# Kernel optimization log

Measured on AMD Instinct MI355X. Metric: run time of the kernel, lower is better.

The kernel has to match this reference:

```python
import jax, jax.numpy as jnp
import numpy as np

N = 50000
EPS = 1e-5


def gcn_conv(x, W, b, src, dst, n):
    # x: [n, Cin]; W: [Cin, Cout]; src/dst: [E+n] with self-loops included
    h = x @ W  # dense GEMM
    deg = jax.ops.segment_sum(jnp.ones_like(dst, dtype=h.dtype), dst, num_segments=n)
    dinv = jnp.where(deg > 0, jax.lax.rsqrt(deg), 0.0)
    norm = dinv[src] * dinv[dst]  # [E+n]
    msgs = h[src] * norm[:, None]  # gather + scale
    out = jax.ops.segment_sum(msgs, dst, num_segments=n)  # scatter-add
    return out + b


def batch_norm(x, gamma, beta, mean, var):
    return (x - mean) * jax.lax.rsqrt(var + EPS) * gamma + beta


def setup_inputs() -> dict:
    key = jax.random.key(0)
    ks = jax.random.split(key, 16)
    IN, H, OUT, E = 1280, 256, 500, 1600000
    x = jax.random.normal(ks[0], (N, IN), dtype=jnp.float32)
    edge_index = jax.random.randint(ks[1], (2, E), 0, N, dtype=jnp.int64)
    def lin(k, cin, cout):
        return jax.random.normal(k, (cin, cout), dtype=jnp.float32) / np.sqrt(cin)
    return {
        "x": x,
        "edge_index": edge_index,
        "W1": lin(ks[2], IN, H), "b1": jnp.zeros((H,), jnp.float32),
        "g1": jnp.ones((H,), jnp.float32), "be1": jnp.zeros((H,), jnp.float32),
        "m1": 0.1 * jax.random.normal(ks[3], (H,), jnp.float32),
        "v1": 0.5 + jax.random.uniform(ks[4], (H,), jnp.float32),
        "W2": lin(ks[5], H, H), "b2": jnp.zeros((H,), jnp.float32),
        "g2": jnp.ones((H,), jnp.float32), "be2": jnp.zeros((H,), jnp.float32),
        "m2": 0.1 * jax.random.normal(ks[6], (H,), jnp.float32),
        "v2": 0.5 + jax.random.uniform(ks[7], (H,), jnp.float32),
        "W3": lin(ks[8], H, OUT), "b3": jnp.zeros((OUT,), jnp.float32),
    }


def reference(x, edge_index, W1, b1, g1, be1, m1, v1, W2, b2, g2, be2, m2, v2, W3, b3):
    n = x.shape[0]
    loops = jnp.arange(n, dtype=edge_index.dtype)
    src = jnp.concatenate([edge_index[0], loops])
    dst = jnp.concatenate([edge_index[1], loops])
    h = gcn_conv(x, W1, b1, src, dst, n)
    h = jax.nn.relu(batch_norm(h, g1, be1, m1, v1))
    h = gcn_conv(h, W2, b2, src, dst, n)
    h = jax.nn.relu(batch_norm(h, g2, be2, m2, v2))
    return gcn_conv(h, W3, b3, src, dst, n)
```

## Files before the change

### kernel.cpp

```cpp
#include <hip/hip_runtime.h>
#include <hip/hip_bf16.h>
#include <stdint.h>

typedef __attribute__((ext_vector_type(4))) float f32x4;
typedef __attribute__((ext_vector_type(8))) short s16x8;
typedef __attribute__((ext_vector_type(4))) unsigned short u16x4;

#define EPSBN 1e-5f

__device__ __forceinline__ float bf2f(unsigned short u) {
  union { unsigned int i; float f; } w; w.i = ((unsigned int)u) << 16; return w.f;
}
__device__ __forceinline__ unsigned short f2bf(float f) {
  __hip_bfloat16 h = __float2bfloat16(f);
  unsigned short u; __builtin_memcpy(&u, &h, 2); return u;
}
__device__ __forceinline__ void gld_lds16(const void* g, void* l) {
  __builtin_amdgcn_global_load_lds(
      (const __attribute__((address_space(1))) void*)(g),
      (__attribute__((address_space(3))) void*)(l), 16, 0, 0);
}

__global__ void k_count(const int* __restrict__ dst, unsigned* __restrict__ deg, int E) {
  int i = blockIdx.x * 256 + threadIdx.x;
  if (i < E) atomicAdd(&deg[dst[i]], 1u);
}
__global__ void k_prep2(const unsigned* __restrict__ deg, float* __restrict__ dinv,
                        unsigned* __restrict__ bsum, int n) {
  __shared__ unsigned s[256];
  int t = threadIdx.x, i = blockIdx.x * 256 + t;
  unsigned d = (i < n) ? deg[i] + 1u : 0u;
  if (i < n) dinv[i] = rsqrtf((float)d);
  s[t] = d;
  __syncthreads();
  for (int st = 128; st > 0; st >>= 1) {
    if (t < st) s[t] += s[t + st];
    __syncthreads();
  }
  if (t == 0) bsum[blockIdx.x] = s[0];
}
__global__ void k_scan_top(const unsigned* __restrict__ bsum, unsigned* __restrict__ bpre,
                           int nb, unsigned* __restrict__ offs, int n) {
  __shared__ unsigned s[256];
  int t = threadIdx.x;
  unsigned v = (t < nb) ? bsum[t] : 0u;
  s[t] = v; __syncthreads();
  for (int d = 1; d < 256; d <<= 1) {
    unsigned a = (t >= d) ? s[t - d] : 0u;
    __syncthreads();
    s[t] += a;
    __syncthreads();
  }
  bpre[t] = s[t] - v;
  if (t == 255) offs[n] = s[255];
}
__global__ void k_scan_fin(const unsigned* __restrict__ deg, const unsigned* __restrict__ bpre,
                           unsigned* __restrict__ offs, unsigned* __restrict__ cur, int n) {
  __shared__ unsigned s[256];
  int t = threadIdx.x, i = blockIdx.x * 256 + t;
  unsigned v = (i < n) ? deg[i] + 1u : 0u;
  s[t] = v; __syncthreads();
  for (int d = 1; d < 256; d <<= 1) {
    unsigned a = (t >= d) ? s[t - d] : 0u;
    __syncthreads();
    s[t] += a;
    __syncthreads();
  }
  if (i < n) {
    unsigned o = bpre[blockIdx.x] + s[t] - v;
    offs[i] = o; cur[i] = o;
  }
}
__global__ void k_fill(const int* __restrict__ src, const int* __restrict__ dst,
                       unsigned* __restrict__ cur, unsigned short* __restrict__ ewp,
                       int E, int n) {
  int i = blockIdx.x * 256 + threadIdx.x;
  int s, d;
  if (i < E)          { s = src[i]; d = dst[i]; }
  else if (i < E + n) { s = d = i - E; }
  else return;
  unsigned p = atomicAdd(&cur[d], 1u);
  ewp[p] = (unsigned short)s;
}
__global__ __launch_bounds__(256) void k_sortw(const unsigned* __restrict__ offs,
                                               unsigned short* __restrict__ ewp, int nN) {
  int wv = (blockIdx.x * 256 + threadIdx.x) >> 6;
  int lane = threadIdx.x & 63;
  if (wv >= nN) return;
  unsigned beg = offs[wv], end = offs[wv + 1];
  int len = (int)(end - beg);
  if (len > 64) return;
  int k = (lane < len) ? (int)ewp[beg + lane] : 0x10000;
#pragma unroll
  for (int size = 2; size <= 64; size <<= 1) {
#pragma unroll
    for (int stride = size >> 1; stride > 0; stride >>= 1) {
      int other = __shfl_xor(k, stride);
      bool up = (lane & size) == 0;
      bool lower = (lane & stride) == 0;
      k = (lower == up) ? min(k, other) : max(k, other);
    }
  }
  if (lane < len) ewp[beg + lane] = (unsigned short)k;
}
__global__ void k_wt3(const float* __restrict__ W1, unsigned short* __restrict__ Wt1,
                      const float* __restrict__ W2, unsigned short* __restrict__ Wt2,
                      const float* __restrict__ W3, unsigned short* __restrict__ Wt3,
                      unsigned short* __restrict__ bufA, unsigned short* __restrict__ bufB,
                      int nN) {
  const int n1 = 256 * 1280, n2 = 256 * 256, n3 = 512 * 256;
  int idx = blockIdx.x * 256 + threadIdx.x;
  if (idx >= n1 + n2 + n3) {
    int z = idx - (n1 + n2 + n3);
    if (z < 256)      bufA[(size_t)nN * 256 + z] = 0;
    else if (z < 512) bufB[(size_t)nN * 256 + (z - 256)] = 0;
    return;
  }
  const float* W; unsigned short* Wt; int K, N;
  if (idx < n1)           { W = W1; Wt = Wt1; K = 1280; N = 256; }
  else if (idx < n1 + n2) { W = W2; Wt = Wt2; K = 256;  N = 256; idx -= n1; }
  else                    { W = W3; Wt = Wt3; K = 256;  N = 500; idx -= n1 + n2; }
  int nn = idx / K, k = idx - nn * K;
  float v = (nn < N) ? W[(size_t)k * N + nn] : 0.f;
  Wt[idx] = f2bf(v);
}

#define BM 128
#define BN 128
#define BK 64

template<int OUTMODE>
__global__ __launch_bounds__(256, 4) void k_gemm(
    const unsigned short* __restrict__ Au, const unsigned short* __restrict__ Bt,
    void* __restrict__ Coutv, const float* __restrict__ bias,
    const float* __restrict__ dinv, int M, int N, int K, int MT, int NT)
{
  __shared__ __align__(16) unsigned short As[BM * BK];
  __shared__ __align__(16) unsigned short Bs[BN * BK];

  int d = blockIdx.x;
  int xc = d & 7, sb = d >> 3;
  int nt = sb % NT, mt = (sb / NT) * 8 + xc;
  if (mt >= MT) return;
  int m0 = mt * BM, n0 = nt * BN;

  int tid = threadIdx.x, lane = tid & 63, wave = tid >> 6;
  int wm = wave >> 1, wn = wave & 1;
  int l15 = lane & 15, l4 = lane >> 4;

  f32x4 acc[4][4];
#pragma unroll
  for (int i = 0; i < 4; ++i)
#pragma unroll
    for (int j = 0; j < 4; ++j) acc[i][j] = 0.f;

  int srow[4], scg[4];
#pragma unroll
  for (int i = 0; i < 4; ++i) {
    int ci = (wave + 4 * i) * 64 + lane;
    srow[i] = ci >> 3;
    scg[i] = (ci & 7) ^ (srow[i] & 7);
  }

  int nk = K / BK;
  for (int kt = 0; kt < nk; ++kt) {
    __syncthreads();
#pragma unroll
    for (int i = 0; i < 4; ++i) {
      int gr = m0 + srow[i]; gr = gr < M ? gr : M - 1;
      gld_lds16(Au + (size_t)gr * K + kt * BK + scg[i] * 8, As + (wave + 4 * i) * 512);
    }
#pragma unroll
    for (int i = 0; i < 4; ++i) {
      int gn = n0 + srow[i];
      gld_lds16(Bt + (size_t)gn * K + kt * BK + scg[i] * 8, Bs + (wave + 4 * i) * 512);
    }
    __syncthreads();

#pragma unroll
    for (int ks = 0; ks < 2; ++ks) {
      s16x8 af[4], bf[4];
#pragma unroll
      for (int f = 0; f < 4; ++f) {
        int r = wm * 64 + f * 16 + l15;
        int ca = (ks * 4 + l4) ^ (r & 7);
        af[f] = *(const s16x8*)(As + r * 64 + ca * 8);
        int nloc = wn * 64 + f * 16 + l15;
        int cb = (ks * 4 + l4) ^ (nloc & 7);
        bf[f] = *(const s16x8*)(Bs + nloc * 64 + cb * 8);
      }
#pragma unroll
      for (int fm = 0; fm < 4; ++fm)
#pragma unroll
        for (int fn = 0; fn < 4; ++fn)
          acc[fm][fn] = __builtin_amdgcn_mfma_f32_16x16x32_bf16(af[fm], bf[fn], acc[fm][fn], 0, 0, 0);
    }
  }

#pragma unroll
  for (int fm = 0; fm < 4; ++fm) {
#pragma unroll
    for (int r = 0; r < 4; ++r) {
      int row = m0 + wm * 64 + fm * 16 + l4 * 4 + r;
      float dsc = (OUTMODE == 0 && row < M) ? dinv[row] : 0.f;
#pragma unroll
      for (int fn = 0; fn < 4; ++fn) {
        int col = n0 + wn * 64 + fn * 16 + l15;
        if (row < M && col < N) {
          if (OUTMODE == 1)
            ((float*)Coutv)[(size_t)row * N + col] = acc[fm][fn][r] + bias[col];
          else
            ((unsigned short*)Coutv)[(size_t)row * N + col] = f2bf(acc[fm][fn][r] * dsc);
        }
      }
    }
  }
}

__global__ __launch_bounds__(256, 3) void k_gemmF(
    const float* __restrict__ Af, const unsigned short* __restrict__ Bt,
    unsigned short* __restrict__ Cout, const float* __restrict__ dinv,
    int M, int N, int K, int MT, int NT)
{
  __shared__ __align__(16) float As[BM * BK];
  __shared__ __align__(16) unsigned short Bs[BN * BK];

  int d = blockIdx.x;
  int xc = d & 7, sb = d >> 3;
  int nt = sb % NT, mt = (sb / NT) * 8 + xc;
  if (mt >= MT) return;
  int m0 = mt * BM, n0 = nt * BN;

  int tid = threadIdx.x, lane = tid & 63, wave = tid >> 6;
  int wm = wave >> 1, wn = wave & 1;
  int l15 = lane & 15, l4 = lane >> 4;

  f32x4 acc[4][4];
#pragma unroll
  for (int i = 0; i < 4; ++i)
#pragma unroll
    for (int j = 0; j < 4; ++j) acc[i][j] = 0.f;

  int arow[8], acs[8];
#pragma unroll
  for (int i = 0; i < 8; ++i) {
    int ci = (i * 4 + wave) * 64 + lane;
    arow[i] = ci >> 4;
    acs[i] = (ci & 15) ^ ((arow[i] & 7) << 1);
  }
  int brow[4], bcg[4];
#pragma unroll
  for (int i = 0; i < 4; ++i) {
    int ci = (i * 4 + wave) * 64 + lane;
    brow[i] = ci >> 3;
    bcg[i] = (ci & 7) ^ (brow[i] & 7);
  }

  int nk = K / BK;
  for (int kt = 0; kt < nk; ++kt) {
    __syncthreads();
#pragma unroll
    for (int i = 0; i < 8; ++i) {
      int gr = m0 + arow[i]; gr = gr < M ? gr : M - 1;
      gld_lds16(Af + (size_t)gr * K + kt * BK + acs[i] * 4, As + (i * 4 + wave) * 256);
    }
#pragma unroll
    for (int i = 0; i < 4; ++i) {
      int gn = n0 + brow[i];
      gld_lds16(Bt + (size_t)gn * K + kt * BK + bcg[i] * 8, Bs + (i * 4 + wave) * 512);
    }
    __syncthreads();

#pragma unroll
    for (int ks = 0; ks < 2; ++ks) {
      s16x8 af[4], bf[4];
#pragma unroll
      for (int f = 0; f < 4; ++f) {
        int r = wm * 64 + f * 16 + l15;
        int c0 = (2 * (ks * 4 + l4)) ^ ((r & 7) << 1);
        f32x4 a0 = *(const f32x4*)(As + r * 64 + c0 * 4);
        f32x4 a1 = *(const f32x4*)(As + r * 64 + c0 * 4 + 4);
        s16x8 pk;
        pk[0] = (short)f2bf(a0[0]); pk[1] = (short)f2bf(a0[1]);
        pk[2] = (short)f2bf(a0[2]); pk[3] = (short)f2bf(a0[3]);
        pk[4] = (short)f2bf(a1[0]); pk[5] = (short)f2bf(a1[1]);
        pk[6] = (short)f2bf(a1[2]); pk[7] = (short)f2bf(a1[3]);
        af[f] = pk;
        int nloc = wn * 64 + f * 16 + l15;
        int cb = (ks * 4 + l4) ^ (nloc & 7);
        bf[f] = *(const s16x8*)(Bs + nloc * 64 + cb * 8);
      }
#pragma unroll
      for (int fm = 0; fm < 4; ++fm)
#pragma unroll
        for (int fn = 0; fn < 4; ++fn)
          acc[fm][fn] = __builtin_amdgcn_mfma_f32_16x16x32_bf16(af[fm], bf[fn], acc[fm][fn], 0, 0, 0);
    }
  }

#pragma unroll
  for (int fm = 0; fm < 4; ++fm) {
#pragma unroll
    for (int r = 0; r < 4; ++r) {
      int row = m0 + wm * 64 + fm * 16 + l4 * 4 + r;
      float dsc = (row < M) ? dinv[row] : 0.f;
#pragma unroll
      for (int fn = 0; fn < 4; ++fn) {
        int col = n0 + wn * 64 + fn * 16 + l15;
        if (row < M && col < N)
          Cout[(size_t)row * N + col] = f2bf(acc[fm][fn][r] * dsc);
      }
    }
  }
}

template<int BNRELU, int SCALEOUT>
__global__ __launch_bounds__(256) void k_agg(
    const unsigned short* __restrict__ h, const unsigned short* __restrict__ ewp,
    const unsigned* __restrict__ offs, const float* __restrict__ dinv,
    const float* __restrict__ bias, const float* __restrict__ gam,
    const float* __restrict__ bet, const float* __restrict__ mea,
    const float* __restrict__ var, unsigned short* __restrict__ outp, int nN)
{
  int wave = threadIdx.x >> 6, lane = threadIdx.x & 63;
  int v = blockIdx.x * 4 + wave;
  if (v >= nN) return;
  unsigned beg = offs[v], end = offs[v + 1];
  int len = (int)(end - beg);
  float dv = dinv[v];
  const unsigned short* hb = h + lane * 4;
  float a0 = 0, a1 = 0, a2 = 0, a3 = 0;

  for (int base = 0; base < len; base += 64) {
    int m = min(64, len - base);
    int myp = (lane < m) ? (int)ewp[beg + base + lane] : nN;
    int ng = (m + 15) >> 4;

    u16x4 q[16];
#pragma unroll
    for (int r = 0; r < 16; ++r) {
      int s = __shfl(myp, r);
      q[r] = *(const u16x4*)(hb + (size_t)s * 256);
    }
    for (int g = 1; g < ng; ++g) {
      u16x4 q2[16];
#pragma unroll
      for (int r = 0; r < 16; ++r) {
        int s = __shfl(myp, g * 16 + r);
        q2[r] = *(const u16x4*)(hb + (size_t)s * 256);
      }
#pragma unroll
      for (int r = 0; r < 16; ++r) {
        a0 += bf2f(q[r][0]); a1 += bf2f(q[r][1]);
        a2 += bf2f(q[r][2]); a3 += bf2f(q[r][3]);
      }
#pragma unroll
      for (int r = 0; r < 16; ++r) q[r] = q2[r];
    }
#pragma unroll
    for (int r = 0; r < 16; ++r) {
      a0 += bf2f(q[r][0]); a1 += bf2f(q[r][1]);
      a2 += bf2f(q[r][2]); a3 += bf2f(q[r][3]);
    }
  }

  float va[4] = {a0, a1, a2, a3};
  int ch0 = lane * 4;
#pragma unroll
  for (int j = 0; j < 4; ++j) {
    int ch = ch0 + j;
    float val = va[j] * dv;
    if (BNRELU) {
      val += bias[ch];
      val = (val - mea[ch]) * rsqrtf(var[ch] + EPSBN) * gam[ch] + bet[ch];
      val = fmaxf(val, 0.f);
    }
    if (SCALEOUT) val *= dv;
    outp[(size_t)v * 256 + ch] = f2bf(val);
  }
}

extern "C" void kernel_launch(void* const* d_in, const int* in_sizes, int n_in,
                              void* d_out, int out_size, void* d_ws, size_t ws_size,
                              hipStream_t stream) {
  const float* x   = (const float*)d_in[0];
  const int*   ei  = (const int*)d_in[1];
  const float* W1  = (const float*)d_in[2];
  const float* b1  = (const float*)d_in[3];
  const float* g1  = (const float*)d_in[4];
  const float* be1 = (const float*)d_in[5];
  const float* m1  = (const float*)d_in[6];
  const float* v1  = (const float*)d_in[7];
  const float* W2  = (const float*)d_in[8];
  const float* b2  = (const float*)d_in[9];
  const float* g2  = (const float*)d_in[10];
  const float* be2 = (const float*)d_in[11];
  const float* m2  = (const float*)d_in[12];
  const float* v2  = (const float*)d_in[13];
  const float* W3  = (const float*)d_in[14];
  const float* b3  = (const float*)d_in[15];

  const int IN = 1280, H = 256, OUT = 500, OUTP = 512;
  int E  = in_sizes[1] / 2;
  int nN = in_sizes[0] / IN;
  const int* srcI = ei;
  const int* dstI = ei + E;

  char* p = (char*)d_ws;
  auto carve = [&](size_t bytes) { char* r = p; p += (bytes + 511) & ~(size_t)511; return r; };
  unsigned short* Wt1 = (unsigned short*)carve((size_t)H * IN * 2);
  unsigned short* Wt2 = (unsigned short*)carve((size_t)H * H * 2);
  unsigned short* Wt3 = (unsigned short*)carve((size_t)OUTP * H * 2);
  unsigned* deg  = (unsigned*)carve((size_t)nN * 4);
  float*    dinv = (float*)carve((size_t)nN * 4);
  unsigned* offs = (unsigned*)carve((size_t)(nN + 1) * 4);
  unsigned* cur  = (unsigned*)carve((size_t)nN * 4);
  unsigned* bsum = (unsigned*)carve(256 * 4);
  unsigned* bpre = (unsigned*)carve(256 * 4);
  unsigned short* ewp = (unsigned short*)carve((size_t)(E + nN) * 2);
  unsigned short* bufA = (unsigned short*)carve((size_t)(nN + 1) * H * 2);
  unsigned short* bufB = (unsigned short*)carve((size_t)(nN + 1) * H * 2);

  hipMemsetAsync(deg, 0, (size_t)nN * 4, stream);

  int NB = (nN + 255) / 256;
  k_count<<<(E + 255) / 256, 256, 0, stream>>>(dstI, deg, E);
  k_prep2<<<NB, 256, 0, stream>>>(deg, dinv, bsum, nN);
  k_scan_top<<<1, 256, 0, stream>>>(bsum, bpre, NB, offs, nN);
  k_scan_fin<<<NB, 256, 0, stream>>>(deg, bpre, offs, cur, nN);
  k_fill<<<(E + nN + 255) / 256, 256, 0, stream>>>(srcI, dstI, cur, ewp, E, nN);
  k_sortw<<<(nN + 3) / 4, 256, 0, stream>>>(offs, ewp, nN);
  k_wt3<<<(256 * 1280 + 256 * 256 + 512 * 256 + 512 + 255) / 256, 256, 0, stream>>>(
      W1, Wt1, W2, Wt2, W3, Wt3, bufA, bufB, nN);

  int MT = (nN + BM - 1) / BM;
  int mg = (MT + 7) / 8;
  int nAgg = (nN + 3) / 4;

  k_gemmF<<<mg * 8 * 2, 256, 0, stream>>>(x, Wt1, bufA, dinv, nN, H, IN, MT, 2);
  k_agg<1, 0><<<nAgg, 256, 0, stream>>>(bufA, ewp, offs, dinv, b1, g1, be1, m1, v1, bufB, nN);
  k_gemm<0><<<mg * 8 * 2, 256, 0, stream>>>(bufB, Wt2, bufA, nullptr, dinv, nN, H, H, MT, 2);
  k_agg<1, 1><<<nAgg, 256, 0, stream>>>(bufA, ewp, offs, dinv, b2, g2, be2, m2, v2, bufB, nN);
  k_agg<0, 0><<<nAgg, 256, 0, stream>>>(bufB, ewp, offs, dinv, nullptr, nullptr, nullptr,
                                        nullptr, nullptr, bufA, nN);
  k_gemm<1><<<mg * 8 * 4, 256, 0, stream>>>(bufA, Wt3, d_out, b3, nullptr, nN, OUT, H, MT, 4);
}
```

Measured before the change: 698.8 us.

## Widen GEMM tiles to 128x256 with 512-thread blocks covering full N

Both GEMM kernels now use a 128x256 output tile computed by 8 waves (512 threads), so one block covers the whole hidden width of 256 and each A row-tile is loaded from global memory once instead of twice. This matters most for the first layer, where A is the large fp32 input read directly. The grouped tile-swizzle scheduling is replaced by a simple linear block index. The fp32 A tile's LDS swizzle gains an extra bit to avoid bank conflicts with the new thread-to-row mapping. In exchange there are fewer and larger blocks with more LDS per block, which reduces occupancy and tail balance, and the output layer still pads 500 columns up to 512.

```diff
diff --git a/kernel.cpp b/kernel.cpp
--- a/kernel.cpp
+++ b/kernel.cpp
@@ -126,26 +126,25 @@
 }
 
 #define BM 128
-#define BN 128
+#define BN 256
 #define BK 64
 
 template<int OUTMODE>
-__global__ __launch_bounds__(256, 4) void k_gemm(
+__global__ __launch_bounds__(512, 6) void k_gemm(
     const unsigned short* __restrict__ Au, const unsigned short* __restrict__ Bt,
     void* __restrict__ Coutv, const float* __restrict__ bias,
-    const float* __restrict__ dinv, int M, int N, int K, int MT, int NT)
+    const float* __restrict__ dinv, int M, int N, int K, int NT)
 {
   __shared__ __align__(16) unsigned short As[BM * BK];
   __shared__ __align__(16) unsigned short Bs[BN * BK];
 
   int d = blockIdx.x;
-  int xc = d & 7, sb = d >> 3;
-  int nt = sb % NT, mt = (sb / NT) * 8 + xc;
-  if (mt >= MT) return;
+  int nt = (NT == 2) ? (d & 1) : 0;
+  int mt = (NT == 2) ? (d >> 1) : d;
   int m0 = mt * BM, n0 = nt * BN;
 
   int tid = threadIdx.x, lane = tid & 63, wave = tid >> 6;
-  int wm = wave >> 1, wn = wave & 1;
+  int wm = wave >> 2, wn = wave & 3;
   int l15 = lane & 15, l4 = lane >> 4;
 
   f32x4 acc[4][4];
@@ -154,26 +153,35 @@
 #pragma unroll
     for (int j = 0; j < 4; ++j) acc[i][j] = 0.f;
 
-  int srow[4], scg[4];
+  int arow[2], acg[2];
+#pragma unroll
+  for (int i = 0; i < 2; ++i) {
+    int ci = i * 512 + tid;
+    arow[i] = ci >> 3;
+    acg[i] = (ci & 7) ^ (arow[i] & 7);
+  }
+  int brow[4], bcg[4];
 #pragma unroll
   for (int i = 0; i < 4; ++i) {
-    int ci = (wave + 4 * i) * 64 + lane;
-    srow[i] = ci >> 3;
-    scg[i] = (ci & 7) ^ (srow[i] & 7);
+    int ci = i * 512 + tid;
+    brow[i] = ci >> 3;
+    bcg[i] = (ci & 7) ^ (brow[i] & 7);
   }
 
   int nk = K / BK;
   for (int kt = 0; kt < nk; ++kt) {
     __syncthreads();
 #pragma unroll
+    for (int i = 0; i < 2; ++i) {
+      int gr = m0 + arow[i]; gr = gr < M ? gr : M - 1;
+      gld_lds16(Au + (size_t)gr * K + kt * BK + acg[i] * 8,
+                As + (size_t)(i * 512 + wave * 64) * 8);
+    }
+#pragma unroll
     for (int i = 0; i < 4; ++i) {
-      int gr = m0 + srow[i]; gr = gr < M ? gr : M - 1;
-      gld_lds16(Au + (size_t)gr * K + kt * BK + scg[i] * 8, As + (wave + 4 * i) * 512);
-    }
-#pragma unroll
-    for (int i = 0; i < 4; ++i) {
-      int gn = n0 + srow[i];
-      gld_lds16(Bt + (size_t)gn * K + kt * BK + scg[i] * 8, Bs + (wave + 4 * i) * 512);
+      int gn = n0 + brow[i];
+      gld_lds16(Bt + (size_t)gn * K + kt * BK + bcg[i] * 8,
+                Bs + (size_t)(i * 512 + wave * 64) * 8);
     }
     __syncthreads();
 
@@ -217,22 +225,19 @@
   }
 }
 
-__global__ __launch_bounds__(256, 3) void k_gemmF(
+__global__ __launch_bounds__(512, 4) void k_gemmF(
     const float* __restrict__ Af, const unsigned short* __restrict__ Bt,
     unsigned short* __restrict__ Cout, const float* __restrict__ dinv,
-    int M, int N, int K, int MT, int NT)
+    int M, int N, int K)
 {
   __shared__ __align__(16) float As[BM * BK];
   __shared__ __align__(16) unsigned short Bs[BN * BK];
 
-  int d = blockIdx.x;
-  int xc = d & 7, sb = d >> 3;
-  int nt = sb % NT, mt = (sb / NT) * 8 + xc;
-  if (mt >= MT) return;
-  int m0 = mt * BM, n0 = nt * BN;
+  int mt = blockIdx.x;
+  int m0 = mt * BM, n0 = 0;
 
   int tid = threadIdx.x, lane = tid & 63, wave = tid >> 6;
-  int wm = wave >> 1, wn = wave & 1;
+  int wm = wave >> 2, wn = wave & 3;
   int l15 = lane & 15, l4 = lane >> 4;
 
   f32x4 acc[4][4];
@@ -241,17 +246,18 @@
 #pragma unroll
     for (int j = 0; j < 4; ++j) acc[i][j] = 0.f;
 
-  int arow[8], acs[8];
-#pragma unroll
-  for (int i = 0; i < 8; ++i) {
-    int ci = (i * 4 + wave) * 64 + lane;
+  int arow[4], acs[4];
+#pragma unroll
+  for (int i = 0; i < 4; ++i) {
+    int ci = i * 512 + tid;
     arow[i] = ci >> 4;
-    acs[i] = (ci & 15) ^ ((arow[i] & 7) << 1);
+    int s = ((arow[i] & 7) << 1) | ((arow[i] >> 3) & 1);
+    acs[i] = (ci & 15) ^ s;
   }
   int brow[4], bcg[4];
 #pragma unroll
   for (int i = 0; i < 4; ++i) {
-    int ci = (i * 4 + wave) * 64 + lane;
+    int ci = i * 512 + tid;
     brow[i] = ci >> 3;
     bcg[i] = (ci & 7) ^ (brow[i] & 7);
   }
@@ -260,14 +266,16 @@
   for (int kt = 0; kt < nk; ++kt) {
     __syncthreads();
 #pragma unroll
-    for (int i = 0; i < 8; ++i) {
+    for (int i = 0; i < 4; ++i) {
       int gr = m0 + arow[i]; gr = gr < M ? gr : M - 1;
-      gld_lds16(Af + (size_t)gr * K + kt * BK + acs[i] * 4, As + (i * 4 + wave) * 256);
+      gld_lds16(Af + (size_t)gr * K + kt * BK + acs[i] * 4,
+                As + (size_t)(i * 512 + wave * 64) * 4);
     }
 #pragma unroll
     for (int i = 0; i < 4; ++i) {
       int gn = n0 + brow[i];
-      gld_lds16(Bt + (size_t)gn * K + kt * BK + bcg[i] * 8, Bs + (i * 4 + wave) * 512);
+      gld_lds16(Bt + (size_t)gn * K + kt * BK + bcg[i] * 8,
+                Bs + (size_t)(i * 512 + wave * 64) * 8);
     }
     __syncthreads();
 
@@ -277,9 +285,10 @@
 #pragma unroll
       for (int f = 0; f < 4; ++f) {
         int r = wm * 64 + f * 16 + l15;
-        int c0 = (2 * (ks * 4 + l4)) ^ ((r & 7) << 1);
-        f32x4 a0 = *(const f32x4*)(As + r * 64 + c0 * 4);
-        f32x4 a1 = *(const f32x4*)(As + r * 64 + c0 * 4 + 4);
+        int s = ((r & 7) << 1) | ((r >> 3) & 1);
+        int gc0 = ks * 8 + 2 * l4;
+        f32x4 a0 = *(const f32x4*)(As + r * 64 + (gc0 ^ s) * 4);
+        f32x4 a1 = *(const f32x4*)(As + r * 64 + ((gc0 + 1) ^ s) * 4);
         s16x8 pk;
         pk[0] = (short)f2bf(a0[0]); pk[1] = (short)f2bf(a0[1]);
         pk[2] = (short)f2bf(a0[2]); pk[3] = (short)f2bf(a0[3]);
@@ -434,14 +443,13 @@
       W1, Wt1, W2, Wt2, W3, Wt3, bufA, bufB, nN);
 
   int MT = (nN + BM - 1) / BM;
-  int mg = (MT + 7) / 8;
   int nAgg = (nN + 3) / 4;
 
-  k_gemmF<<<mg * 8 * 2, 256, 0, stream>>>(x, Wt1, bufA, dinv, nN, H, IN, MT, 2);
+  k_gemmF<<<MT, 512, 0, stream>>>(x, Wt1, bufA, dinv, nN, H, IN);
   k_agg<1, 0><<<nAgg, 256, 0, stream>>>(bufA, ewp, offs, dinv, b1, g1, be1, m1, v1, bufB, nN);
-  k_gemm<0><<<mg * 8 * 2, 256, 0, stream>>>(bufB, Wt2, bufA, nullptr, dinv, nN, H, H, MT, 2);
+  k_gemm<0><<<MT, 512, 0, stream>>>(bufB, Wt2, bufA, nullptr, dinv, nN, H, H, 1);
   k_agg<1, 1><<<nAgg, 256, 0, stream>>>(bufA, ewp, offs, dinv, b2, g2, be2, m2, v2, bufB, nN);
   k_agg<0, 0><<<nAgg, 256, 0, stream>>>(bufB, ewp, offs, dinv, nullptr, nullptr, nullptr,
                                         nullptr, nullptr, bufA, nN);
-  k_gemm<1><<<mg * 8 * 4, 256, 0, stream>>>(bufA, Wt3, d_out, b3, nullptr, nN, OUT, H, MT, 4);
-}
+  k_gemm<1><<<MT * 2, 512, 0, stream>>>(bufA, Wt3, d_out, b3, nullptr, nN, OUT, H, 2);
+}
```

After: 835.3 us. +19.5%, slower.

## Widen first-layer GEMM tile to full 256 columns with 512-thread blocks

Applied to the files above, without the earlier changes.

The fp32-input first GEMM now uses 512-thread blocks that each cover a 128x256 output tile spanning the whole hidden width. Each fp32 A tile is therefore loaded from global memory and converted to bf16 once instead of twice, removing the duplicated read of the large x matrix. The LDS swizzle for A changes to fold in an extra row bit. The trade-off is more LDS and registers per block, which lowers occupancy and leaves fewer, larger blocks.

```diff
diff --git a/kernel.cpp b/kernel.cpp
--- a/kernel.cpp
+++ b/kernel.cpp
@@ -126,7 +126,6 @@
 }
 
 #define BM 128
-#define BN 128
 #define BK 64
 
 template<int OUTMODE>
@@ -136,13 +135,13 @@
     const float* __restrict__ dinv, int M, int N, int K, int MT, int NT)
 {
   __shared__ __align__(16) unsigned short As[BM * BK];
-  __shared__ __align__(16) unsigned short Bs[BN * BK];
+  __shared__ __align__(16) unsigned short Bs[128 * BK];
 
   int d = blockIdx.x;
   int xc = d & 7, sb = d >> 3;
   int nt = sb % NT, mt = (sb / NT) * 8 + xc;
   if (mt >= MT) return;
-  int m0 = mt * BM, n0 = nt * BN;
+  int m0 = mt * BM, n0 = nt * 128;
 
   int tid = threadIdx.x, lane = tid & 63, wave = tid >> 6;
   int wm = wave >> 1, wn = wave & 1;
@@ -217,22 +216,19 @@
   }
 }
 
-__global__ __launch_bounds__(256, 3) void k_gemmF(
+__global__ __launch_bounds__(512, 4) void k_gemmF(
     const float* __restrict__ Af, const unsigned short* __restrict__ Bt,
     unsigned short* __restrict__ Cout, const float* __restrict__ dinv,
-    int M, int N, int K, int MT, int NT)
+    int M, int N, int K)
 {
   __shared__ __align__(16) float As[BM * BK];
-  __shared__ __align__(16) unsigned short Bs[BN * BK];
-
-  int d = blockIdx.x;
-  int xc = d & 7, sb = d >> 3;
-  int nt = sb % NT, mt = (sb / NT) * 8 + xc;
-  if (mt >= MT) return;
-  int m0 = mt * BM, n0 = nt * BN;
+  __shared__ __align__(16) unsigned short Bs[256 * BK];
+
+  int mt = blockIdx.x;
+  int m0 = mt * BM, n0 = 0;
 
   int tid = threadIdx.x, lane = tid & 63, wave = tid >> 6;
-  int wm = wave >> 1, wn = wave & 1;
+  int wm = wave >> 2, wn = wave & 3;
   int l15 = lane & 15, l4 = lane >> 4;
 
   f32x4 acc[4][4];
@@ -241,17 +237,18 @@
 #pragma unroll
     for (int j = 0; j < 4; ++j) acc[i][j] = 0.f;
 
-  int arow[8], acs[8];
-#pragma unroll
-  for (int i = 0; i < 8; ++i) {
-    int ci = (i * 4 + wave) * 64 + lane;
+  int arow[4], acs[4];
+#pragma unroll
+  for (int i = 0; i < 4; ++i) {
+    int ci = i * 512 + tid;
     arow[i] = ci >> 4;
-    acs[i] = (ci & 15) ^ ((arow[i] & 7) << 1);
+    int s = ((arow[i] & 7) << 1) | ((arow[i] >> 3) & 1);
+    acs[i] = (ci & 15) ^ s;
   }
   int brow[4], bcg[4];
 #pragma unroll
   for (int i = 0; i < 4; ++i) {
-    int ci = (i * 4 + wave) * 64 + lane;
+    int ci = i * 512 + tid;
     brow[i] = ci >> 3;
     bcg[i] = (ci & 7) ^ (brow[i] & 7);
   }
@@ -260,14 +257,16 @@
   for (int kt = 0; kt < nk; ++kt) {
     __syncthreads();
 #pragma unroll
-    for (int i = 0; i < 8; ++i) {
+    for (int i = 0; i < 4; ++i) {
       int gr = m0 + arow[i]; gr = gr < M ? gr : M - 1;
-      gld_lds16(Af + (size_t)gr * K + kt * BK + acs[i] * 4, As + (i * 4 + wave) * 256);
+      gld_lds16(Af + (size_t)gr * K + kt * BK + acs[i] * 4,
+                As + (size_t)(i * 512 + wave * 64) * 4);
     }
 #pragma unroll
     for (int i = 0; i < 4; ++i) {
       int gn = n0 + brow[i];
-      gld_lds16(Bt + (size_t)gn * K + kt * BK + bcg[i] * 8, Bs + (i * 4 + wave) * 512);
+      gld_lds16(Bt + (size_t)gn * K + kt * BK + bcg[i] * 8,
+                Bs + (size_t)(i * 512 + wave * 64) * 8);
     }
     __syncthreads();
 
@@ -277,9 +276,10 @@
 #pragma unroll
       for (int f = 0; f < 4; ++f) {
         int r = wm * 64 + f * 16 + l15;
-        int c0 = (2 * (ks * 4 + l4)) ^ ((r & 7) << 1);
-        f32x4 a0 = *(const f32x4*)(As + r * 64 + c0 * 4);
-        f32x4 a1 = *(const f32x4*)(As + r * 64 + c0 * 4 + 4);
+        int s = ((r & 7) << 1) | ((r >> 3) & 1);
+        int gc0 = ks * 8 + 2 * l4;
+        f32x4 a0 = *(const f32x4*)(As + r * 64 + (gc0 ^ s) * 4);
+        f32x4 a1 = *(const f32x4*)(As + r * 64 + ((gc0 + 1) ^ s) * 4);
         s16x8 pk;
         pk[0] = (short)f2bf(a0[0]); pk[1] = (short)f2bf(a0[1]);
         pk[2] = (short)f2bf(a0[2]); pk[3] = (short)f2bf(a0[3]);
@@ -437,7 +437,7 @@
   int mg = (MT + 7) / 8;
   int nAgg = (nN + 3) / 4;
 
-  k_gemmF<<<mg * 8 * 2, 256, 0, stream>>>(x, Wt1, bufA, dinv, nN, H, IN, MT, 2);
+  k_gemmF<<<MT, 512, 0, stream>>>(x, Wt1, bufA, dinv, nN, H, IN);
   k_agg<1, 0><<<nAgg, 256, 0, stream>>>(bufA, ewp, offs, dinv, b1, g1, be1, m1, v1, bufB, nN);
   k_gemm<0><<<mg * 8 * 2, 256, 0, stream>>>(bufB, Wt2, bufA, nullptr, dinv, nN, H, H, MT, 2);
   k_agg<1, 1><<<nAgg, 256, 0, stream>>>(bufA, ewp, offs, dinv, b2, g2, be2, m2, v2, bufB, nN);
```

Result: no change. 687.9 us (-1.6%).
